# Performance work log

Measured on AMD Instinct MI355X. Metric: run time of the kernel, lower is better.

## Reference

```python
import jax, jax.numpy as jnp
import numpy as np

B, IN, NC, O, H = 256, 2048, 1000, 4096, 4  # batch, in_features, num_classes, n_decoders, hidden
NEG_SLOPE = 0.1

def setup_inputs() -> dict:
    key = jax.random.key(0)
    ks = jax.random.split(key, 7)
    s1 = 1.0 / np.sqrt(IN)
    s2 = 1.0 / np.sqrt(H)
    return {
        "x":   jax.random.normal(ks[0], (B, IN), jnp.float32),
        "fcW": jax.random.normal(ks[1], (NC, IN), jnp.float32) * s1,
        "fcb": jax.random.normal(ks[2], (NC,), jnp.float32) * s1,
        "W1":  jax.random.normal(ks[3], (O, IN, H), jnp.float32) * s1,
        "b1":  jax.random.normal(ks[4], (O, H), jnp.float32) * s1,
        "W2":  jax.random.normal(ks[5], (O, H), jnp.float32) * s2,
        "b2":  jax.random.normal(ks[6], (O,), jnp.float32) * s2,
    }

def reference(x, fcW, fcb, W1, b1, W2, b2):
    # fc head: x1 = x @ fcW^T + fcb  -> [B, NC]
    x1 = jnp.einsum("bi,ci->bc", x, fcW) + fcb
    # 4096 tiny MLPs batched into one grouped GEMM:
    # h = leaky_relu(x @ W1_o + b1_o) for each decoder o  -> [B, O, H]
    h = jnp.einsum("bi,oih->boh", x, W1) + b1
    h = jnp.where(h >= 0, h, NEG_SLOPE * h)
    # second layer (H->1) collapses to a weighted reduction -> [B, O]
    x2 = jnp.einsum("boh,oh->bo", h, W2) + b2
    return (x1, x2)
```

## Files before the change

### kernel.cpp

```cpp
#include <hip/hip_runtime.h>


typedef __bf16 bf16_t;
typedef __bf16 bf16x4 __attribute__((ext_vector_type(4)));
typedef __bf16 bf16x8 __attribute__((ext_vector_type(8)));
typedef float  f32x4  __attribute__((ext_vector_type(4)));
typedef float  f32x16 __attribute__((ext_vector_type(16)));

__global__ __launch_bounds__(256, 2)
void fused_dual(const float* __restrict__ x,
                const float* __restrict__ fcW,
                const float* __restrict__ fcb,
                const float* __restrict__ W1,
                const float* __restrict__ b1,
                const float* __restrict__ W2,
                const float* __restrict__ b2,
                float* __restrict__ out)
{
    __shared__ __align__(16) char lA[128 * 128];
    __shared__ __align__(16) char lB[64 * 128];

    const int tid  = threadIdx.x;
    const int lane = tid & 63, w = tid >> 6;
    const int l31  = lane & 31, half = lane >> 5;

    const int idx = blockIdx.x;
    const int wid = (idx & 7) * 68 + (idx >> 3);
    const int cg  = wid >> 1, rg = wid & 1, m0 = rg * 128;
    const bool is_fc = (cg < 16);
    const int c0  = (is_fc ? cg : cg - 16) * 64;

    const int arow = tid >> 2;
    const int aq   = tid & 3;
    const float* aBase = x + (m0 + arow) * 2048 + aq * 4;

    const float* bBase;
    if (is_fc) {
        int rowc = c0 + arow; if (rowc > 999) rowc = 999;
        bBase = fcW + rowc * 2048 + aq * 4;
    } else {
        bBase = W1 + ((c0 >> 2) + w * 4) * 8192 + lane * 4;
    }

    f32x4 aR[8], bR[4];

    auto LOAD = [&](int kt) {
        const float* ap = aBase + kt * 64;
        #pragma unroll
        for (int j = 0; j < 8; ++j)
            aR[j] = *(const f32x4*)(ap + (j & 1) * (64 * 2048) + (j >> 1) * 16);
        if (is_fc) {
            const float* bp = bBase + kt * 64;
            #pragma unroll
            for (int j = 0; j < 4; ++j) bR[j] = *(const f32x4*)(bp + j * 16);
        } else {
            const float* bp = bBase + kt * 256;
            #pragma unroll
            for (int q = 0; q < 4; ++q) bR[q] = *(const f32x4*)(bp + q * 8192);
        }
    };

    auto STAGE = [&]() {
        #pragma unroll
        for (int j = 0; j < 8; ++j) {
            const int r  = arow + 64 * (j & 1);
            const int kb = aq * 8 + (j >> 1) * 32;
            const int ad = r * 128 + (((kb >> 4) ^ (r & 7)) << 4) + (kb & 15);
            bf16x4 v;
            #pragma unroll
            for (int c = 0; c < 4; ++c) v[c] = (bf16_t)aR[j][c];
            *(bf16x4*)(lA + ad) = v;
        }
        if (is_fc) {
            #pragma unroll
            for (int j = 0; j < 4; ++j) {
                const int kb = aq * 8 + j * 32;
                const int ad = arow * 128 + (((kb >> 4) ^ (arow & 7)) << 4) + (kb & 15);
                bf16x4 v;
                #pragma unroll
                for (int c = 0; c < 4; ++c) v[c] = (bf16_t)bR[j][c];
                *(bf16x4*)(lB + ad) = v;
            }
        } else {
            const int gsub = ((lane >> 3) << 4) + (lane & 7) * 2;
            #pragma unroll
            for (int q = 0; q < 4; ++q)
            #pragma unroll
            for (int h = 0; h < 4; ++h) {
                const int n = w * 16 + q * 4 + h;
                const int ad = n * 128 + (gsub ^ ((n & 7) << 4));
                *(bf16_t*)(lB + ad) = (bf16_t)bR[q][h];
            }
        }
    };

    const int mh = (w & 1) * 64, nh = (w >> 1) * 32;
    f32x16 acc[2];
    #pragma unroll
    for (int i = 0; i < 2; ++i)
        #pragma unroll
        for (int r = 0; r < 16; ++r) acc[i][r] = 0.f;

    LOAD(0);
    for (int kt = 0; kt < 32; ++kt) {
        __syncthreads();
        STAGE();
        __syncthreads();
        if (kt != 31) LOAD(kt + 1);
        const int nrow = nh + l31;
        #pragma unroll
        for (int ks = 0; ks < 4; ++ks) {
            const int g = ks * 2 + half;
            bf16x8 bf = *(const bf16x8*)(lB + nrow * 128 + ((g ^ (nrow & 7)) << 4));
            #pragma unroll
            for (int i = 0; i < 2; ++i) {
                const int mrow = mh + i * 32 + l31;
                bf16x8 af = *(const bf16x8*)(lA + mrow * 128 + ((g ^ (mrow & 7)) << 4));
                acc[i] = __builtin_amdgcn_mfma_f32_32x32x16_bf16(af, bf, acc[i], 0, 0, 0);
            }
        }
    }

    if (is_fc) {
        const int c = c0 + nh + l31;
        const bool valid = (c < 1000);
        const float bias = fcb[valid ? c : 999];
        #pragma unroll
        for (int i = 0; i < 2; ++i)
        #pragma unroll
        for (int r = 0; r < 16; ++r) {
            if (valid) {
                const int m = m0 + mh + i * 32 + (r & 3) + 8 * (r >> 2) + 4 * half;
                out[m * 1000 + c] = acc[i][r] + bias;
            }
        }
    } else {
        float* x2 = out + 256 * 1000;
        const int d = cg - 16;
        const int n_glob = c0 + nh + l31;
        const float b1v = b1[n_glob], w2v = W2[n_glob];
        const float b2v = b2[n_glob >> 2];
        __syncthreads();
        float* xs = (float*)lA;
        const int o_loc = (nh + l31) >> 2;
        #pragma unroll
        for (int i = 0; i < 2; ++i)
        #pragma unroll
        for (int r = 0; r < 16; ++r) {
            float h = acc[i][r] + b1v;
            h = (h >= 0.f) ? h : 0.1f * h;
            float wv = h * w2v;
            wv += __shfl_xor(wv, 1, 64);
            wv += __shfl_xor(wv, 2, 64);
            if ((lane & 3) == 0) {
                const int row = mh + i * 32 + (r & 3) + 8 * (r >> 2) + 4 * half;
                xs[row * 16 + o_loc] = wv + b2v;
            }
        }
        __syncthreads();
        #pragma unroll
        for (int j = 0; j < 2; ++j) {
            const int row = (tid >> 2) + 64 * j, part = tid & 3;
            f32x4 v = *(const f32x4*)(xs + row * 16 + part * 4);
            *(f32x4*)(x2 + (m0 + row) * 4096 + d * 16 + part * 4) = v;
        }
    }
}

extern "C" void kernel_launch(void* const* d_in, const int* in_sizes, int n_in,
                              void* d_out, int out_size, void* d_ws, size_t ws_size,
                              hipStream_t stream)
{
    (void)in_sizes; (void)n_in; (void)d_ws; (void)ws_size; (void)out_size;
    const float* x   = (const float*)d_in[0];
    const float* fcW = (const float*)d_in[1];
    const float* fcb = (const float*)d_in[2];
    const float* W1  = (const float*)d_in[3];
    const float* b1  = (const float*)d_in[4];
    const float* W2  = (const float*)d_in[5];
    const float* b2  = (const float*)d_in[6];
    fused_dual<<<544, 256, 0, stream>>>(x, fcW, fcb, W1, b1, W2, b2, (float*)d_out);
}
```

Measured before the change: 241.5 us.

## Double-buffer LDS with 512-thread blocks and one MFMA tile per wave

Each block now runs 8 waves instead of 4, and each wave computes a single 32x32 MFMA tile, so per-thread register loads and accumulators are halved. LDS is double-buffered: the next tile is staged while the current one is consumed, and the global load runs two tiles ahead. This leaves one barrier per k-step instead of two. The cost is double the LDS per block (48KB), and there are fewer MFMAs per LDS read, which lowers arithmetic intensity per wave.

```diff
diff --git a/kernel.cpp b/kernel.cpp
--- a/kernel.cpp
+++ b/kernel.cpp
@@ -7,7 +7,7 @@
 typedef float  f32x4  __attribute__((ext_vector_type(4)));
 typedef float  f32x16 __attribute__((ext_vector_type(16)));
 
-__global__ __launch_bounds__(256, 2)
+__global__ __launch_bounds__(512, 6)
 void fused_dual(const float* __restrict__ x,
                 const float* __restrict__ fcW,
                 const float* __restrict__ fcb,
@@ -17,8 +17,7 @@
                 const float* __restrict__ b2,
                 float* __restrict__ out)
 {
-    __shared__ __align__(16) char lA[128 * 128];
-    __shared__ __align__(16) char lB[64 * 128];
+    __shared__ __align__(16) char lds[2][24576];
 
     const int tid  = threadIdx.x;
     const int lane = tid & 63, w = tid >> 6;
@@ -30,108 +29,106 @@
     const bool is_fc = (cg < 16);
     const int c0  = (is_fc ? cg : cg - 16) * 64;
 
-    const int arow = tid >> 2;
-    const int aq   = tid & 3;
+    const int arow = tid >> 2, aq = tid & 3;
     const float* aBase = x + (m0 + arow) * 2048 + aq * 4;
 
+    const int brow = tid >> 3, bq = tid & 7;
     const float* bBase;
     if (is_fc) {
-        int rowc = c0 + arow; if (rowc > 999) rowc = 999;
-        bBase = fcW + rowc * 2048 + aq * 4;
+        int rowc = c0 + brow; if (rowc > 999) rowc = 999;
+        bBase = fcW + rowc * 2048 + bq * 8;
     } else {
-        bBase = W1 + ((c0 >> 2) + w * 4) * 8192 + lane * 4;
+        bBase = W1 + ((c0 >> 2) + w * 2) * 8192 + lane * 4;
     }
 
-    f32x4 aR[8], bR[4];
+    f32x4 aR[4], bR[2];
 
     auto LOAD = [&](int kt) {
         const float* ap = aBase + kt * 64;
         #pragma unroll
-        for (int j = 0; j < 8; ++j)
-            aR[j] = *(const f32x4*)(ap + (j & 1) * (64 * 2048) + (j >> 1) * 16);
+        for (int j = 0; j < 4; ++j) aR[j] = *(const f32x4*)(ap + j * 16);
         if (is_fc) {
             const float* bp = bBase + kt * 64;
-            #pragma unroll
-            for (int j = 0; j < 4; ++j) bR[j] = *(const f32x4*)(bp + j * 16);
+            bR[0] = *(const f32x4*)(bp);
+            bR[1] = *(const f32x4*)(bp + 4);
         } else {
             const float* bp = bBase + kt * 256;
-            #pragma unroll
-            for (int q = 0; q < 4; ++q) bR[q] = *(const f32x4*)(bp + q * 8192);
+            bR[0] = *(const f32x4*)(bp);
+            bR[1] = *(const f32x4*)(bp + 8192);
         }
     };
 
-    auto STAGE = [&]() {
+    auto STAGE = [&](int p) {
+        char* lA = lds[p];
+        char* lB = lds[p] + 16384;
         #pragma unroll
-        for (int j = 0; j < 8; ++j) {
-            const int r  = arow + 64 * (j & 1);
-            const int kb = aq * 8 + (j >> 1) * 32;
-            const int ad = r * 128 + (((kb >> 4) ^ (r & 7)) << 4) + (kb & 15);
+        for (int j = 0; j < 4; ++j) {
+            const int kb = aq * 8 + j * 32;
+            const int ad = arow * 128 + (((kb >> 4) ^ (arow & 7)) << 4) + (kb & 15);
             bf16x4 v;
             #pragma unroll
             for (int c = 0; c < 4; ++c) v[c] = (bf16_t)aR[j][c];
             *(bf16x4*)(lA + ad) = v;
         }
         if (is_fc) {
+            const int ad = brow * 128 + ((bq ^ (brow & 7)) << 4);
+            bf16x8 v;
             #pragma unroll
-            for (int j = 0; j < 4; ++j) {
-                const int kb = aq * 8 + j * 32;
-                const int ad = arow * 128 + (((kb >> 4) ^ (arow & 7)) << 4) + (kb & 15);
-                bf16x4 v;
-                #pragma unroll
-                for (int c = 0; c < 4; ++c) v[c] = (bf16_t)bR[j][c];
-                *(bf16x4*)(lB + ad) = v;
-            }
+            for (int c = 0; c < 4; ++c) { v[c] = (bf16_t)bR[0][c]; v[4 + c] = (bf16_t)bR[1][c]; }
+            *(bf16x8*)(lB + ad) = v;
         } else {
             const int gsub = ((lane >> 3) << 4) + (lane & 7) * 2;
             #pragma unroll
-            for (int q = 0; q < 4; ++q)
+            for (int q = 0; q < 2; ++q)
             #pragma unroll
             for (int h = 0; h < 4; ++h) {
-                const int n = w * 16 + q * 4 + h;
+                const int n = w * 8 + q * 4 + h;
                 const int ad = n * 128 + (gsub ^ ((n & 7) << 4));
                 *(bf16_t*)(lB + ad) = (bf16_t)bR[q][h];
             }
         }
     };
 
-    const int mh = (w & 1) * 64, nh = (w >> 1) * 32;
-    f32x16 acc[2];
+    const int mh = (w & 3) * 32, nh = (w >> 2) * 32;
+    f32x16 acc;
     #pragma unroll
-    for (int i = 0; i < 2; ++i)
-        #pragma unroll
-        for (int r = 0; r < 16; ++r) acc[i][r] = 0.f;
+    for (int r = 0; r < 16; ++r) acc[r] = 0.f;
 
     LOAD(0);
+    STAGE(0);
+    LOAD(1);
+    asm volatile("s_waitcnt lgkmcnt(0)" ::: "memory");
+    __builtin_amdgcn_s_barrier();
+    asm volatile("" ::: "memory");
+
+    const int mrow = mh + l31, nrow = nh + l31;
+    #pragma unroll 2
     for (int kt = 0; kt < 32; ++kt) {
-        __syncthreads();
-        STAGE();
-        __syncthreads();
-        if (kt != 31) LOAD(kt + 1);
-        const int nrow = nh + l31;
+        const int p = kt & 1;
+        const char* lA = lds[p];
+        const char* lB = lds[p] + 16384;
         #pragma unroll
         for (int ks = 0; ks < 4; ++ks) {
             const int g = ks * 2 + half;
             bf16x8 bf = *(const bf16x8*)(lB + nrow * 128 + ((g ^ (nrow & 7)) << 4));
-            #pragma unroll
-            for (int i = 0; i < 2; ++i) {
-                const int mrow = mh + i * 32 + l31;
-                bf16x8 af = *(const bf16x8*)(lA + mrow * 128 + ((g ^ (mrow & 7)) << 4));
-                acc[i] = __builtin_amdgcn_mfma_f32_32x32x16_bf16(af, bf, acc[i], 0, 0, 0);
-            }
+            bf16x8 af = *(const bf16x8*)(lA + mrow * 128 + ((g ^ (mrow & 7)) << 4));
+            acc = __builtin_amdgcn_mfma_f32_32x32x16_bf16(af, bf, acc, 0, 0, 0);
         }
+        if (kt < 31) STAGE(p ^ 1);
+        if (kt < 30) LOAD(kt + 2);
+        asm volatile("s_waitcnt lgkmcnt(0)" ::: "memory");
+        __builtin_amdgcn_s_barrier();
+        asm volatile("" ::: "memory");
     }
 
     if (is_fc) {
         const int c = c0 + nh + l31;
-        const bool valid = (c < 1000);
-        const float bias = fcb[valid ? c : 999];
-        #pragma unroll
-        for (int i = 0; i < 2; ++i)
-        #pragma unroll
-        for (int r = 0; r < 16; ++r) {
-            if (valid) {
-                const int m = m0 + mh + i * 32 + (r & 3) + 8 * (r >> 2) + 4 * half;
-                out[m * 1000 + c] = acc[i][r] + bias;
+        if (c < 1000) {
+            const float bias = fcb[c];
+            #pragma unroll
+            for (int r = 0; r < 16; ++r) {
+                const int m = m0 + mh + (r & 3) + 8 * (r >> 2) + 4 * half;
+                out[m * 1000 + c] = acc[r] + bias;
             }
         }
     } else {
@@ -140,30 +137,26 @@
         const int n_glob = c0 + nh + l31;
         const float b1v = b1[n_glob], w2v = W2[n_glob];
         const float b2v = b2[n_glob >> 2];
-        __syncthreads();
-        float* xs = (float*)lA;
+        float* xs = (float*)lds;
         const int o_loc = (nh + l31) >> 2;
         #pragma unroll
-        for (int i = 0; i < 2; ++i)
-        #pragma unroll
         for (int r = 0; r < 16; ++r) {
-            float h = acc[i][r] + b1v;
+            float h = acc[r] + b1v;
             h = (h >= 0.f) ? h : 0.1f * h;
             float wv = h * w2v;
             wv += __shfl_xor(wv, 1, 64);
             wv += __shfl_xor(wv, 2, 64);
             if ((lane & 3) == 0) {
-                const int row = mh + i * 32 + (r & 3) + 8 * (r >> 2) + 4 * half;
+                const int row = mh + (r & 3) + 8 * (r >> 2) + 4 * half;
                 xs[row * 16 + o_loc] = wv + b2v;
             }
         }
-        __syncthreads();
-        #pragma unroll
-        for (int j = 0; j < 2; ++j) {
-            const int row = (tid >> 2) + 64 * j, part = tid & 3;
-            f32x4 v = *(const f32x4*)(xs + row * 16 + part * 4);
-            *(f32x4*)(x2 + (m0 + row) * 4096 + d * 16 + part * 4) = v;
-        }
+        asm volatile("s_waitcnt lgkmcnt(0)" ::: "memory");
+        __builtin_amdgcn_s_barrier();
+        asm volatile("" ::: "memory");
+        const int row = tid >> 2, part = tid & 3;
+        f32x4 v = *(const f32x4*)(xs + row * 16 + part * 4);
+        *(f32x4*)(x2 + (m0 + row) * 4096 + d * 16 + part * 4) = v;
     }
 }
 
@@ -179,5 +172,5 @@
     const float* b1  = (const float*)d_in[4];
     const float* W2  = (const float*)d_in[5];
     const float* b2  = (const float*)d_in[6];
-    fused_dual<<<544, 256, 0, stream>>>(x, fcW, fcb, W1, b1, W2, b2, (float*)d_out);
+    fused_dual<<<544, 512, 0, stream>>>(x, fcW, fcb, W1, b1, W2, b2, (float*)d_out);
 }
```

After: 254.7 us. 5.5% more time.

## Prepack x and fcW to bf16 tiles, double-buffer LDS with direct global-to-LDS loads

Applied to the files above, without the earlier changes.

Adds a pre-pass kernel that converts x and fcW into swizzled bf16 tiles in the workspace. The main kernel then streams those tiles straight into LDS with global_load_lds, using a double buffer and one barrier per k-step. W1 is still loaded through registers and written to the alternate buffer after the MFMAs. The aim is to cut the fp32 load volume, the conversion work and the barrier stalls in the GEMM loop, at the cost of an extra launch, workspace traffic and more LDS per block, with occupancy raised to 3 blocks per unit.

```diff
diff --git a/kernel.cpp b/kernel.cpp
--- a/kernel.cpp
+++ b/kernel.cpp
@@ -7,18 +7,67 @@
 typedef float  f32x4  __attribute__((ext_vector_type(4)));
 typedef float  f32x16 __attribute__((ext_vector_type(16)));
 
-__global__ __launch_bounds__(256, 2)
-void fused_dual(const float* __restrict__ x,
-                const float* __restrict__ fcW,
+#define GLDS(gp, lp) __builtin_amdgcn_global_load_lds( \
+    (const __attribute__((address_space(1))) void*)(gp), \
+    (__attribute__((address_space(3))) void*)(lp), 16, 0, 0)
+
+#define WS_A_OFF 0
+#define WS_F_OFF (64 * 16384)
+
+__global__ __launch_bounds__(256)
+void pack_tiles(const float* __restrict__ x, const float* __restrict__ fcW,
+                char* __restrict__ ws)
+{
+    const int tid = threadIdx.x;
+    const int bid = blockIdx.x;
+    if (bid < 64) {
+        const int rg = bid >> 5, kt = bid & 31;
+        char* dst = ws + WS_A_OFF + (size_t)bid * 16384;
+        #pragma unroll
+        for (int i = 0; i < 4; ++i) {
+            const int gi = tid + 256 * i;
+            const int r = gi >> 3, s = gi & 7, g = s ^ (r & 7);
+            const float* sp = x + (size_t)(rg * 128 + r) * 2048 + kt * 64 + g * 8;
+            f32x4 v0 = *(const f32x4*)sp, v1 = *(const f32x4*)(sp + 4);
+            bf16x8 o;
+            #pragma unroll
+            for (int c = 0; c < 4; ++c) { o[c] = (bf16_t)v0[c]; o[4 + c] = (bf16_t)v1[c]; }
+            *(bf16x8*)(dst + r * 128 + s * 16) = o;
+        }
+    } else {
+        const int t = bid - 64;
+        const int cg = t >> 5, kt = t & 31;
+        char* dst = ws + WS_F_OFF + (size_t)t * 8192;
+        #pragma unroll
+        for (int i = 0; i < 2; ++i) {
+            const int gi = tid + 256 * i;
+            const int n = gi >> 3, s = gi & 7, g = s ^ ((n >> 2) & 7);
+            const int c = cg * 64 + n;
+            bf16x8 o;
+            if (c < 1000) {
+                const float* sp = fcW + (size_t)c * 2048 + kt * 64 + g * 8;
+                f32x4 v0 = *(const f32x4*)sp, v1 = *(const f32x4*)(sp + 4);
+                #pragma unroll
+                for (int cc = 0; cc < 4; ++cc) { o[cc] = (bf16_t)v0[cc]; o[4 + cc] = (bf16_t)v1[cc]; }
+            } else {
+                #pragma unroll
+                for (int cc = 0; cc < 8; ++cc) o[cc] = (bf16_t)0.f;
+            }
+            *(bf16x8*)(dst + n * 128 + s * 16) = o;
+        }
+    }
+}
+
+__global__ __launch_bounds__(256, 3)
+void fused_dual(const char* __restrict__ ws,
+                const float* __restrict__ W1,
                 const float* __restrict__ fcb,
-                const float* __restrict__ W1,
                 const float* __restrict__ b1,
                 const float* __restrict__ W2,
                 const float* __restrict__ b2,
                 float* __restrict__ out)
 {
-    __shared__ __align__(16) char lA[128 * 128];
-    __shared__ __align__(16) char lB[64 * 128];
+    __shared__ __align__(16) char lds[2][24576];
 
     const int tid  = threadIdx.x;
     const int lane = tid & 63, w = tid >> 6;
@@ -29,69 +78,50 @@
     const int cg  = wid >> 1, rg = wid & 1, m0 = rg * 128;
     const bool is_fc = (cg < 16);
     const int c0  = (is_fc ? cg : cg - 16) * 64;
-
-    const int arow = tid >> 2;
-    const int aq   = tid & 3;
-    const float* aBase = x + (m0 + arow) * 2048 + aq * 4;
-
-    const float* bBase;
-    if (is_fc) {
-        int rowc = c0 + arow; if (rowc > 999) rowc = 999;
-        bBase = fcW + rowc * 2048 + aq * 4;
-    } else {
-        bBase = W1 + ((c0 >> 2) + w * 4) * 8192 + lane * 4;
-    }
-
-    f32x4 aR[8], bR[4];
-
-    auto LOAD = [&](int kt) {
-        const float* ap = aBase + kt * 64;
-        #pragma unroll
-        for (int j = 0; j < 8; ++j)
-            aR[j] = *(const f32x4*)(ap + (j & 1) * (64 * 2048) + (j >> 1) * 16);
-        if (is_fc) {
-            const float* bp = bBase + kt * 64;
-            #pragma unroll
-            for (int j = 0; j < 4; ++j) bR[j] = *(const f32x4*)(bp + j * 16);
-        } else {
-            const float* bp = bBase + kt * 256;
-            #pragma unroll
-            for (int q = 0; q < 4; ++q) bR[q] = *(const f32x4*)(bp + q * 8192);
-        }
-    };
-
-    auto STAGE = [&]() {
-        #pragma unroll
-        for (int j = 0; j < 8; ++j) {
-            const int r  = arow + 64 * (j & 1);
-            const int kb = aq * 8 + (j >> 1) * 32;
-            const int ad = r * 128 + (((kb >> 4) ^ (r & 7)) << 4) + (kb & 15);
+    const int dcg = is_fc ? 0 : (cg - 16);
+
+    const char* aT = ws + WS_A_OFF + (size_t)rg * 32 * 16384;
+    const char* bT = ws + WS_F_OFF + (size_t)cg * 32 * 8192;
+
+    const int lo = lane * 16;
+
+    const int u    = tid & 127, hi = tid >> 7;
+    const int oloc = u >> 3, gg = u & 7;
+    const int slot = gg ^ (oloc & 7);
+    const float* w1Base = W1 + (size_t)(dcg * 16 + oloc) * 8192
+                             + (gg * 8 + hi * 4) * 4;
+    const int wbase = (4 * oloc) * 128 + slot * 16 + hi * 8;
+
+    f32x4 bReg[4];
+
+    auto B_LOAD = [&](int kt) {
+        const float* p = w1Base + kt * 256;
+        #pragma unroll
+        for (int j = 0; j < 4; ++j) bReg[j] = *(const f32x4*)(p + j * 4);
+    };
+    auto B_WRITE = [&](int pbuf) {
+        char* lB = &lds[pbuf][16384];
+        #pragma unroll
+        for (int h = 0; h < 4; ++h) {
             bf16x4 v;
             #pragma unroll
-            for (int c = 0; c < 4; ++c) v[c] = (bf16_t)aR[j][c];
-            *(bf16x4*)(lA + ad) = v;
-        }
-        if (is_fc) {
-            #pragma unroll
-            for (int j = 0; j < 4; ++j) {
-                const int kb = aq * 8 + j * 32;
-                const int ad = arow * 128 + (((kb >> 4) ^ (arow & 7)) << 4) + (kb & 15);
-                bf16x4 v;
-                #pragma unroll
-                for (int c = 0; c < 4; ++c) v[c] = (bf16_t)bR[j][c];
-                *(bf16x4*)(lB + ad) = v;
-            }
-        } else {
-            const int gsub = ((lane >> 3) << 4) + (lane & 7) * 2;
-            #pragma unroll
-            for (int q = 0; q < 4; ++q)
-            #pragma unroll
-            for (int h = 0; h < 4; ++h) {
-                const int n = w * 16 + q * 4 + h;
-                const int ad = n * 128 + (gsub ^ ((n & 7) << 4));
-                *(bf16_t*)(lB + ad) = (bf16_t)bR[q][h];
-            }
-        }
+            for (int j = 0; j < 4; ++j) v[j] = (bf16_t)bReg[j][h];
+            *(bf16x4*)(lB + wbase + h * 128) = v;
+        }
+    };
+    auto GLDS_A = [&](int kt, int pbuf) {
+        char* lA = &lds[pbuf][0];
+        const char* ga = aT + kt * 16384 + w * 4096;
+        #pragma unroll
+        for (int i = 0; i < 4; ++i)
+            GLDS(ga + i * 1024 + lo, lA + w * 4096 + i * 1024);
+    };
+    auto GLDS_B_FC = [&](int kt, int pbuf) {
+        char* lB = &lds[pbuf][16384];
+        const char* gb = bT + kt * 8192 + w * 2048;
+        #pragma unroll
+        for (int i = 0; i < 2; ++i)
+            GLDS(gb + i * 1024 + lo, lB + w * 2048 + i * 1024);
     };
 
     const int mh = (w & 1) * 64, nh = (w >> 1) * 32;
@@ -101,17 +131,27 @@
         #pragma unroll
         for (int r = 0; r < 16; ++r) acc[i][r] = 0.f;
 
-    LOAD(0);
+    if (is_fc) {
+        GLDS_A(0, 0); GLDS_B_FC(0, 0);
+    } else {
+        B_LOAD(0); GLDS_A(0, 0); B_WRITE(0);
+    }
+    __syncthreads();
+
+    const int nrow = nh + l31;
+    const int bro  = nrow * 128 + (((nrow >> 2) & 7) << 4);
     for (int kt = 0; kt < 32; ++kt) {
-        __syncthreads();
-        STAGE();
-        __syncthreads();
-        if (kt != 31) LOAD(kt + 1);
-        const int nrow = nh + l31;
+        const int p = kt & 1;
+        if (kt < 31) {
+            if (is_fc) { GLDS_A(kt + 1, p ^ 1); GLDS_B_FC(kt + 1, p ^ 1); }
+            else       { B_LOAD(kt + 1); GLDS_A(kt + 1, p ^ 1); }
+        }
+        const char* lA = &lds[p][0];
+        const char* lB = &lds[p][16384];
         #pragma unroll
         for (int ks = 0; ks < 4; ++ks) {
             const int g = ks * 2 + half;
-            bf16x8 bf = *(const bf16x8*)(lB + nrow * 128 + ((g ^ (nrow & 7)) << 4));
+            bf16x8 bf = *(const bf16x8*)(lB + (bro ^ (g << 4)));
             #pragma unroll
             for (int i = 0; i < 2; ++i) {
                 const int mrow = mh + i * 32 + l31;
@@ -119,17 +159,18 @@
                 acc[i] = __builtin_amdgcn_mfma_f32_32x32x16_bf16(af, bf, acc[i], 0, 0, 0);
             }
         }
+        if (!is_fc && kt < 31) B_WRITE(p ^ 1);
+        __syncthreads();
     }
 
     if (is_fc) {
         const int c = c0 + nh + l31;
-        const bool valid = (c < 1000);
-        const float bias = fcb[valid ? c : 999];
-        #pragma unroll
-        for (int i = 0; i < 2; ++i)
-        #pragma unroll
-        for (int r = 0; r < 16; ++r) {
-            if (valid) {
+        if (c < 1000) {
+            const float bias = fcb[c];
+            #pragma unroll
+            for (int i = 0; i < 2; ++i)
+            #pragma unroll
+            for (int r = 0; r < 16; ++r) {
                 const int m = m0 + mh + i * 32 + (r & 3) + 8 * (r >> 2) + 4 * half;
                 out[m * 1000 + c] = acc[i][r] + bias;
             }
@@ -140,8 +181,7 @@
         const int n_glob = c0 + nh + l31;
         const float b1v = b1[n_glob], w2v = W2[n_glob];
         const float b2v = b2[n_glob >> 2];
-        __syncthreads();
-        float* xs = (float*)lA;
+        float* xs = (float*)lds;
         const int o_loc = (nh + l31) >> 2;
         #pragma unroll
         for (int i = 0; i < 2; ++i)
@@ -171,7 +211,7 @@
                               void* d_out, int out_size, void* d_ws, size_t ws_size,
                               hipStream_t stream)
 {
-    (void)in_sizes; (void)n_in; (void)d_ws; (void)ws_size; (void)out_size;
+    (void)in_sizes; (void)n_in; (void)out_size; (void)ws_size;
     const float* x   = (const float*)d_in[0];
     const float* fcW = (const float*)d_in[1];
     const float* fcb = (const float*)d_in[2];
@@ -179,5 +219,7 @@
     const float* b1  = (const float*)d_in[4];
     const float* W2  = (const float*)d_in[5];
     const float* b2  = (const float*)d_in[6];
-    fused_dual<<<544, 256, 0, stream>>>(x, fcW, fcb, W1, b1, W2, b2, (float*)d_out);
+    char* ws = (char*)d_ws;
+    pack_tiles<<<576, 256, 0, stream>>>(x, fcW, ws);
+    fused_dual<<<544, 256, 0, stream>>>(ws, W1, fcb, b1, W2, b2, (float*)d_out);
 }
```

After: 254.7 us. 1.05x slower.
